# Kernel tuning notes

Measured on AMD Instinct MI355X. Metric: run time of the kernel, lower is better.

## Reference

```python
import jax, jax.numpy as jnp
import numpy as np

B, K, C = 32, 512, 32  # batch, node count (spatial size), hardcoded out channels


def setup_inputs() -> dict:
    key = jax.random.key(0)
    k1, k2, k3, k4, k5 = jax.random.split(key, 5)
    x = jax.random.normal(k1, (B, 1, K, K), dtype=jnp.float32)
    # torch Conv2d default init: U(-1/sqrt(fan_in), 1/sqrt(fan_in)), fan_in = 1*K
    s = 1.0 / np.sqrt(K).astype(np.float32)
    w_col = jax.random.uniform(k2, (C, K), jnp.float32, -s, s)  # Conv2d(1,32,(1,K)) weight
    b_col = jax.random.uniform(k3, (C,), jnp.float32, -s, s)
    w_row = jax.random.uniform(k4, (C, K), jnp.float32, -s, s)  # Conv2d(1,32,(K,1)) weight
    b_row = jax.random.uniform(k5, (C,), jnp.float32, -s, s)
    return {"input": x, "w_col": w_col, "b_col": b_col, "w_row": w_row, "b_row": b_row}


def reference(input, w_col, b_col, w_row, b_row):
    x = input[:, 0]  # [B,K,K]
    # conv_column: kernel (1,K) -> per-row dot with w_col -> [B,C,K] (spatial [K,1] squeezed)
    col = jnp.einsum('bik,ok->boi', x, w_col) + b_col[None, :, None]
    # conv_row: kernel (K,1) -> per-column dot with w_row -> [B,C,K] (spatial [1,K] squeezed)
    row = jnp.einsum('bkj,ok->boj', x, w_row) + b_row[None, :, None]
    # cat([conv_row]*K, dim=2) makes every row equal to `row`; cat([conv_column]*K, dim=3)
    # makes every column equal to `col`. Their matmul is the constant dot(row, col)
    # broadcast over the whole KxK output (exactly the original math, reduced).
    s = jnp.einsum('bok,bok->bo', row, col)  # [B,C]
    Bn, Cn = s.shape
    return jnp.broadcast_to(s[:, :, None, None], (Bn, Cn, x.shape[1], x.shape[2]))
```

## Files before the change

### kernel.cpp

```cpp
#include <hip/hip_runtime.h>

#define Bn 32
#define Kn 512
#define Cn 32

typedef float vf4 __attribute__((ext_vector_type(4)));

#define WTC_OFF   0
#define WTR_OFF   16384
#define COL_OFF   32768
#define ROW_OFF   557056
#define S_OFF     1081344

__global__ void k_prep(const float* __restrict__ w_col,
                       const float* __restrict__ w_row,
                       float* __restrict__ ws) {
    if (blockIdx.x == 128) {
        ((vf4*)(ws + S_OFF))[threadIdx.x] = (vf4){0.f, 0.f, 0.f, 0.f};
        return;
    }
    int idx = blockIdx.x * 256 + threadIdx.x;
    int which = idx >> 14;
    int e = idx & 16383;
    int o = e & 31, k = e >> 5;
    const float* src = which ? w_row : w_col;
    float* dst = ws + (which ? WTR_OFF : WTC_OFF);
    dst[e] = src[o * Kn + k];
}

__global__ __launch_bounds__(256) void k_colrow(
    const float* __restrict__ x,
    const float* __restrict__ bcol,
    const float* __restrict__ brow,
    float* __restrict__ ws) {
    const int chunk = blockIdx.x;
    const int b     = blockIdx.y;
    const int phase = blockIdx.z;
    const int t0  = chunk * 64;
    const int tid = threadIdx.x;
    const int t   = tid & 63;
    const int kh  = __builtin_amdgcn_readfirstlane(tid >> 6);

    __shared__ float red[2][64 * 33];

    const float* __restrict__ wT = ws + (phase ? WTR_OFF : WTC_OFF);
    const float* __restrict__ xb = x + b * (Kn * Kn);

    float acc[32];
#pragma unroll
    for (int o = 0; o < 32; ++o) acc[o] = 0.f;

    if (phase == 0) {
        const float4* __restrict__ xr = (const float4*)(xb + (t0 + t) * Kn) + kh * 32;
        const float* __restrict__ wk = wT + kh * 128 * 32;
#pragma unroll 2
        for (int j = 0; j < 32; ++j) {
            float4 v = xr[j];
            const float* __restrict__ w0 = wk + j * 128;
#pragma unroll
            for (int o = 0; o < 32; ++o) acc[o] = fmaf(v.x, w0[o],      acc[o]);
#pragma unroll
            for (int o = 0; o < 32; ++o) acc[o] = fmaf(v.y, w0[32 + o], acc[o]);
#pragma unroll
            for (int o = 0; o < 32; ++o) acc[o] = fmaf(v.z, w0[64 + o], acc[o]);
#pragma unroll
            for (int o = 0; o < 32; ++o) acc[o] = fmaf(v.w, w0[96 + o], acc[o]);
        }
    } else {
        const int kb = kh * 128;
#pragma unroll 4
        for (int k = 0; k < 128; ++k) {
            float xv = xb[(kb + k) * Kn + t0 + t];
            const float* __restrict__ w = wT + (kb + k) * 32;
#pragma unroll
            for (int o = 0; o < 32; ++o) acc[o] = fmaf(xv, w[o], acc[o]);
        }
    }

    __syncthreads();
    if (kh >= 2) {
        float* r = red[kh - 2];
#pragma unroll
        for (int o = 0; o < 32; ++o) r[t * 33 + o] = acc[o];
    }
    __syncthreads();
    if (kh < 2) {
        const float* r = red[kh];
#pragma unroll
        for (int o = 0; o < 32; ++o) acc[o] += r[t * 33 + o];
    }
    __syncthreads();
    if (kh == 1) {
#pragma unroll
        for (int o = 0; o < 32; ++o) red[1][t * 33 + o] = acc[o];
    }
    __syncthreads();
    if (kh == 0) {
        const float* __restrict__ bias = phase ? brow : bcol;
        float* __restrict__ dst = ws + (phase ? ROW_OFF : COL_OFF) + (b * Kn + t0 + t) * 32;
#pragma unroll
        for (int o = 0; o < 32; ++o)
            dst[o] = acc[o] + red[1][t * 33 + o] + bias[o];
    }
}

__global__ void k_reduce(float* __restrict__ ws) {
    const int tg = blockIdx.x & 3, b = blockIdx.x >> 2;
    const int tid = threadIdx.x;
    const int o = tid & 31, tp = tid >> 5;
    const float* __restrict__ cp = ws + COL_OFF + b * (Kn * 32);
    const float* __restrict__ rp = ws + ROW_OFF + b * (Kn * 32);
    const int tbase = tg * 128 + tp * 16;
    float sum = 0.f;
#pragma unroll
    for (int j = 0; j < 16; ++j) {
        int tt = tbase + j;
        sum += cp[tt * 32 + o] * rp[tt * 32 + o];
    }
    __shared__ float red[8 * 33];
    red[tp * 33 + o] = sum;
    __syncthreads();
    if (tid < 32) {
        float s = 0.f;
#pragma unroll
        for (int j = 0; j < 8; ++j) s += red[j * 33 + tid];
        atomicAdd(ws + S_OFF + b * 32 + tid, s);
    }
}

__global__ __launch_bounds__(256) void k_broadcast(const float* __restrict__ ws,
                                                   float* __restrict__ out) {
    const int bo   = blockIdx.x >> 4;
    const int part = blockIdx.x & 15;
    const float sval = ws[S_OFF + bo];
    vf4 v = (vf4){sval, sval, sval, sval};
    vf4* __restrict__ out4 =
        (vf4*)out + (size_t)bo * 65536 + (size_t)part * 4096 + threadIdx.x;
#pragma unroll
    for (int j = 0; j < 16; ++j)
        __builtin_nontemporal_store(v, out4 + j * 256);
}

extern "C" void kernel_launch(void* const* d_in, const int* in_sizes, int n_in,
                              void* d_out, int out_size, void* d_ws, size_t ws_size,
                              hipStream_t stream) {
    const float* x     = (const float*)d_in[0];
    const float* w_col = (const float*)d_in[1];
    const float* b_col = (const float*)d_in[2];
    const float* w_row = (const float*)d_in[3];
    const float* b_row = (const float*)d_in[4];
    float* out = (float*)d_out;
    float* ws  = (float*)d_ws;

    hipLaunchKernelGGL(k_prep, dim3(129), dim3(256), 0, stream, w_col, w_row, ws);
    hipLaunchKernelGGL(k_colrow, dim3(8, 32, 2), dim3(256), 0, stream, x, b_col, b_row, ws);
    hipLaunchKernelGGL(k_reduce, dim3(128), dim3(256), 0, stream, ws);
    hipLaunchKernelGGL(k_broadcast, dim3(16384), dim3(256), 0, stream, ws, out);
}
```

Before: 1.119 ms.

## Fuse column/row projections with dot-product reduction in one kernel

```diff
diff --git a/kernel.cpp b/kernel.cpp
--- a/kernel.cpp
+++ b/kernel.cpp
@@ -8,9 +8,7 @@
 
 #define WTC_OFF   0
 #define WTR_OFF   16384
-#define COL_OFF   32768
-#define ROW_OFF   557056
-#define S_OFF     1081344
+#define S_OFF     32768
 
 __global__ void k_prep(const float* __restrict__ w_col,
                        const float* __restrict__ w_row,
@@ -28,22 +26,22 @@
     dst[e] = src[o * Kn + k];
 }
 
-__global__ __launch_bounds__(256) void k_colrow(
+__global__ __launch_bounds__(512) void k_fused(
     const float* __restrict__ x,
     const float* __restrict__ bcol,
     const float* __restrict__ brow,
     float* __restrict__ ws) {
     const int chunk = blockIdx.x;
     const int b     = blockIdx.y;
-    const int phase = blockIdx.z;
     const int t0  = chunk * 64;
     const int tid = threadIdx.x;
     const int t   = tid & 63;
-    const int kh  = __builtin_amdgcn_readfirstlane(tid >> 6);
+    const int wv  = __builtin_amdgcn_readfirstlane(tid >> 6);
+    const int phase = wv >> 2;
+    const int kh    = wv & 3;
 
-    __shared__ float red[2][64 * 33];
+    __shared__ float buf[8][64 * 33];
 
-    const float* __restrict__ wT = ws + (phase ? WTR_OFF : WTC_OFF);
     const float* __restrict__ xb = x + b * (Kn * Kn);
 
     float acc[32];
@@ -52,7 +50,7 @@
 
     if (phase == 0) {
         const float4* __restrict__ xr = (const float4*)(xb + (t0 + t) * Kn) + kh * 32;
-        const float* __restrict__ wk = wT + kh * 128 * 32;
+        const float* __restrict__ wk = ws + WTC_OFF + kh * 128 * 32;
 #pragma unroll 2
         for (int j = 0; j < 32; ++j) {
             float4 v = xr[j];
@@ -67,63 +65,42 @@
             for (int o = 0; o < 32; ++o) acc[o] = fmaf(v.w, w0[96 + o], acc[o]);
         }
     } else {
+        const float* __restrict__ wr = ws + WTR_OFF;
         const int kb = kh * 128;
 #pragma unroll 4
         for (int k = 0; k < 128; ++k) {
             float xv = xb[(kb + k) * Kn + t0 + t];
-            const float* __restrict__ w = wT + (kb + k) * 32;
+            const float* __restrict__ w = wr + (kb + k) * 32;
 #pragma unroll
             for (int o = 0; o < 32; ++o) acc[o] = fmaf(xv, w[o], acc[o]);
         }
     }
 
-    __syncthreads();
-    if (kh >= 2) {
-        float* r = red[kh - 2];
+    {
+        float* __restrict__ my = buf[wv] + t * 33;
 #pragma unroll
-        for (int o = 0; o < 32; ++o) r[t * 33 + o] = acc[o];
+        for (int o = 0; o < 32; ++o) my[o] = acc[o];
     }
     __syncthreads();
-    if (kh < 2) {
-        const float* r = red[kh];
-#pragma unroll
-        for (int o = 0; o < 32; ++o) acc[o] += r[t * 33 + o];
-    }
-    __syncthreads();
-    if (kh == 1) {
-#pragma unroll
-        for (int o = 0; o < 32; ++o) red[1][t * 33 + o] = acc[o];
-    }
-    __syncthreads();
-    if (kh == 0) {
-        const float* __restrict__ bias = phase ? brow : bcol;
-        float* __restrict__ dst = ws + (phase ? ROW_OFF : COL_OFF) + (b * Kn + t0 + t) * 32;
-#pragma unroll
-        for (int o = 0; o < 32; ++o)
-            dst[o] = acc[o] + red[1][t * 33 + o] + bias[o];
-    }
-}
 
-__global__ void k_reduce(float* __restrict__ ws) {
-    const int tg = blockIdx.x & 3, b = blockIdx.x >> 2;
-    const int tid = threadIdx.x;
-    const int o = tid & 31, tp = tid >> 5;
-    const float* __restrict__ cp = ws + COL_OFF + b * (Kn * 32);
-    const float* __restrict__ rp = ws + ROW_OFF + b * (Kn * 32);
-    const int tbase = tg * 128 + tp * 16;
+    const int o = tid & 31, g = tid >> 5;
+    const float bc = bcol[o], br = brow[o];
     float sum = 0.f;
 #pragma unroll
-    for (int j = 0; j < 16; ++j) {
-        int tt = tbase + j;
-        sum += cp[tt * 32 + o] * rp[tt * 32 + o];
+    for (int j = 0; j < 4; ++j) {
+        const int tt = g * 4 + j;
+        const int a  = tt * 33 + o;
+        float c = buf[0][a] + buf[1][a] + buf[2][a] + buf[3][a] + bc;
+        float r = buf[4][a] + buf[5][a] + buf[6][a] + buf[7][a] + br;
+        sum = fmaf(c, r, sum);
     }
-    __shared__ float red[8 * 33];
-    red[tp * 33 + o] = sum;
+    __shared__ float red2[16 * 33];
+    red2[g * 33 + o] = sum;
     __syncthreads();
     if (tid < 32) {
         float s = 0.f;
 #pragma unroll
-        for (int j = 0; j < 8; ++j) s += red[j * 33 + tid];
+        for (int j = 0; j < 16; ++j) s += red2[j * 33 + tid];
         atomicAdd(ws + S_OFF + b * 32 + tid, s);
     }
 }
@@ -153,7 +130,6 @@
     float* ws  = (float*)d_ws;
 
     hipLaunchKernelGGL(k_prep, dim3(129), dim3(256), 0, stream, w_col, w_row, ws);
-    hipLaunchKernelGGL(k_colrow, dim3(8, 32, 2), dim3(256), 0, stream, x, b_col, b_row, ws);
-    hipLaunchKernelGGL(k_reduce, dim3(128), dim3(256), 0, stream, ws);
+    hipLaunchKernelGGL(k_fused, dim3(8, 32), dim3(512), 0, stream, x, b_col, b_row, ws);
     hipLaunchKernelGGL(k_broadcast, dim3(16384), dim3(256), 0, stream, ws, out);
 }
```

New measurement: 1.102 ms. Within noise of the previous version (-1.6%).
